# Kernel tuning notes

Hardware: AMD Instinct MI355X
Metric: run time of the kernel (lower is better)

## Reference

```python
import jax, jax.numpy as jnp
import numpy as np


def setup_inputs() -> dict:
    key = jax.random.key(0)
    ks = jax.random.split(key, 6)
    B, T, D, U = 32, 2048, 512, 512
    scale = 1.0 / np.sqrt(D)
    return {
        "values": jax.random.normal(ks[0], (B, T, D), dtype=jnp.float32),
        "query": jax.random.normal(ks[1], (B, D), dtype=jnp.float32),
        "W1": jax.random.normal(ks[2], (D, U), dtype=jnp.float32) * scale,
        "b1": jnp.zeros((U,), dtype=jnp.float32),
        "W2": jax.random.normal(ks[3], (D, U), dtype=jnp.float32) * scale,
        "b2": jnp.zeros((U,), dtype=jnp.float32),
        "V": jax.random.normal(ks[4], (U, 1), dtype=jnp.float32) * (1.0 / np.sqrt(U)),
        "bV": jnp.zeros((1,), dtype=jnp.float32),
    }


def reference(values, query, W1, b1, W2, b2, V, bV):
    # values: [B,T,D], query: [B,D]
    proj_v = jnp.einsum("btd,du->btu", values, W1) + b1          # [B,T,U]
    proj_q = (query @ W2 + b2)[:, None, :]                        # [B,1,U]
    score = jnp.tanh(proj_v + proj_q) @ V + bV                    # [B,T,1]
    attention_weights = jax.nn.softmax(score, axis=1)             # [B,T,1]
    context_vector = jnp.sum(attention_weights * values, axis=1)  # [B,D]
    return context_vector, attention_weights
```

## Files before the change

kernel.cpp:

```cpp
#include <hip/hip_runtime.h>
#include <math.h>


#define B_ 32
#define T_ 2048
#define D_ 512
#define U_ 512
#define M_ (B_ * T_)

typedef _Float16 half8 __attribute__((ext_vector_type(8)));
typedef float floatx4 __attribute__((ext_vector_type(4)));

__device__ __forceinline__ float fast_tanh(float x) {
  x = fminf(fmaxf(x, -20.f), 20.f);
  const float e = __expf(2.f * x);
  return 1.f - 2.f / (e + 1.f);
}

__device__ __forceinline__ void load_lds16f(const float* g, float* l) {
  __builtin_amdgcn_global_load_lds(
      (const __attribute__((address_space(1))) void*)g,
      (__attribute__((address_space(3))) void*)l, 16, 0, 0);
}

__global__ __launch_bounds__(256) void prep_fused(
    const float* __restrict__ W1, const float* __restrict__ query,
    const float* __restrict__ W2, const float* __restrict__ b2,
    _Float16* __restrict__ w1t, float* __restrict__ projq,
    float* __restrict__ context) {
  __shared__ float sh[64 * 65];
  const int bx = blockIdx.x;
  const int tid = threadIdx.x;
  if (bx < 64) {
    const int t = bx;
    const int k0 = (t >> 3) * 64, u0 = (t & 7) * 64;
    float(*sm)[65] = (float(*)[65])sh;
    const int lu = tid & 63;
    const int g = tid >> 6;
#pragma unroll
    for (int i = 0; i < 16; ++i) {
      const int row = g * 16 + i;
      sm[row][lu] = W1[(long)(k0 + row) * U_ + u0 + lu];
    }
    __syncthreads();
#pragma unroll
    for (int i = 0; i < 16; ++i) {
      const int row = g * 16 + i;
      w1t[(long)(u0 + row) * D_ + k0 + lu] = (_Float16)sm[lu][row];
    }
  } else {
    const int t = bx - 64;
    const int gid = t * 256 + tid;
    context[gid] = 0.f;
    const int b = t >> 1;
    const int u = (t & 1) * 256 + tid;
    for (int d = tid; d < D_; d += 256) sh[d] = query[b * D_ + d];
    __syncthreads();
    float acc = 0.f;
#pragma unroll 8
    for (int d = 0; d < D_; ++d) acc += sh[d] * W2[d * U_ + u];
    projq[b * U_ + u] = acc + b2[u];
  }
}

__global__ __launch_bounds__(512, 1) void score_fused(
    const float* __restrict__ values, const _Float16* __restrict__ w1t,
    const float* __restrict__ b1, const float* __restrict__ projq,
    const float* __restrict__ V, float* __restrict__ scores) {
  const int m0 = blockIdx.x * 128;
  const int b = blockIdx.x >> 4;
  const int tid = threadIdx.x;
  const int lane = tid & 63;
  const int w = tid >> 6;
  const int wm = (w & 1) * 64;
  const int wu = (w >> 1) * 128;
  const int ln = lane & 15;
  const int lq = lane >> 4;

  __shared__ alignas(16) float As[2][128 * 32];
  __shared__ float red[4][128];

  const int dr = lane >> 3;
  const int dc = (lane & 7) ^ dr;
  const float* gA[2];
#pragma unroll
  for (int j = 0; j < 2; ++j) {
    const int r = w * 16 + j * 8 + dr;
    gA[j] = values + (long)(m0 + r) * D_ + dc * 4;
  }

  const _Float16* bp[8];
#pragma unroll
  for (int ni = 0; ni < 8; ++ni)
    bp[ni] = w1t + (long)(wu + ni * 16 + ln) * D_ + lq * 8;

  floatx4 acc[4][8] = {};

#pragma unroll
  for (int j = 0; j < 2; ++j)
    load_lds16f(gA[j], &As[0][(w * 16 + j * 8) * 32]);
  __syncthreads();

  for (int t = 0; t < 16; ++t) {
    const int p = t & 1;
    half8 bf[8];
#pragma unroll
    for (int ni = 0; ni < 8; ++ni) bf[ni] = *(const half8*)(bp[ni] + t * 32);
    if (t < 15) {
#pragma unroll
      for (int j = 0; j < 2; ++j)
        load_lds16f(gA[j] + (t + 1) * 32,
                    &As[p ^ 1][(w * 16 + j * 8) * 32]);
    }
    half8 af[4];
#pragma unroll
    for (int mi = 0; mi < 4; ++mi) {
      const int r = wm + mi * 16 + ln;
      const float* row = &As[p][r * 32];
      const float4 lo = *(const float4*)(row + (((2 * lq) ^ (r & 7)) * 4));
      const float4 hi = *(const float4*)(row + (((2 * lq + 1) ^ (r & 7)) * 4));
      af[mi] = half8{(_Float16)lo.x, (_Float16)lo.y, (_Float16)lo.z,
                     (_Float16)lo.w, (_Float16)hi.x, (_Float16)hi.y,
                     (_Float16)hi.z, (_Float16)hi.w};
    }
#pragma unroll
    for (int mi = 0; mi < 4; ++mi)
#pragma unroll
      for (int ni = 0; ni < 8; ++ni)
        acc[mi][ni] = __builtin_amdgcn_mfma_f32_16x16x32_f16(
            af[mi], bf[ni], acc[mi][ni], 0, 0, 0);
    __syncthreads();
  }

  float pre[8], vv[8];
#pragma unroll
  for (int ni = 0; ni < 8; ++ni) {
    const int u = wu + ni * 16 + ln;
    pre[ni] = b1[u] + projq[b * U_ + u];
    vv[ni] = V[u];
  }
#pragma unroll
  for (int mi = 0; mi < 4; ++mi) {
#pragma unroll
    for (int r = 0; r < 4; ++r) {
      float t = 0.f;
#pragma unroll
      for (int ni = 0; ni < 8; ++ni)
        t += fast_tanh(acc[mi][ni][r] + pre[ni]) * vv[ni];
      t += __shfl_xor(t, 1);
      t += __shfl_xor(t, 2);
      t += __shfl_xor(t, 4);
      t += __shfl_xor(t, 8);
      if (ln == 0) red[w >> 1][wm + mi * 16 + lq * 4 + r] = t;
    }
  }
  __syncthreads();
  if (tid < 128)
    scores[m0 + tid] =
        red[0][tid] + red[1][tid] + red[2][tid] + red[3][tid];
}

__global__ __launch_bounds__(256) void softmax_context_kernel(
    const float* __restrict__ scores, const float* __restrict__ values,
    float* __restrict__ weights, float* __restrict__ context) {
  const int b = blockIdx.x;
  const int t0 = blockIdx.y * 64;
  const int tid = threadIdx.x;

  float v[8];
  float mx = -INFINITY;
#pragma unroll
  for (int i = 0; i < 8; ++i) {
    v[i] = scores[b * T_ + i * 256 + tid];
    mx = fmaxf(mx, v[i]);
  }
#pragma unroll
  for (int off = 32; off > 0; off >>= 1) mx = fmaxf(mx, __shfl_down(mx, off));
  __shared__ float sm[4], ss[4];
  if ((tid & 63) == 0) sm[tid >> 6] = mx;
  __syncthreads();
  mx = fmaxf(fmaxf(sm[0], sm[1]), fmaxf(sm[2], sm[3]));
  float sum = 0.f;
#pragma unroll
  for (int i = 0; i < 8; ++i) sum += __expf(v[i] - mx);
#pragma unroll
  for (int off = 32; off > 0; off >>= 1) sum += __shfl_down(sum, off);
  if ((tid & 63) == 0) ss[tid >> 6] = sum;
  __syncthreads();
  const float inv = 1.f / (ss[0] + ss[1] + ss[2] + ss[3]);

  __shared__ float wsh[64];
  if (tid < 64) {
    const float ww = __expf(scores[b * T_ + t0 + tid] - mx) * inv;
    wsh[tid] = ww;
    weights[b * T_ + t0 + tid] = ww;
  }
  __syncthreads();

  const int g = tid >> 7;
  const int dx = tid & 127;
  __shared__ float4 part[128];
  float4 acc = make_float4(0.f, 0.f, 0.f, 0.f);
  const float4* vp = (const float4*)(values + (long)(b * T_ + t0 + g) * D_) + dx;
#pragma unroll 4
  for (int t = 0; t < 32; ++t) {
    const float4 x = vp[(long)(2 * t) * (D_ / 4)];
    const float ww = wsh[2 * t + g];
    acc.x += ww * x.x; acc.y += ww * x.y; acc.z += ww * x.z; acc.w += ww * x.w;
  }
  if (g == 0) part[dx] = acc;
  __syncthreads();
  if (g == 1) {
    const float4 p = part[dx];
    atomicAdd(&context[b * D_ + dx * 4 + 0], acc.x + p.x);
    atomicAdd(&context[b * D_ + dx * 4 + 1], acc.y + p.y);
    atomicAdd(&context[b * D_ + dx * 4 + 2], acc.z + p.z);
    atomicAdd(&context[b * D_ + dx * 4 + 3], acc.w + p.w);
  }
}

extern "C" void kernel_launch(void* const* d_in, const int* in_sizes, int n_in,
                              void* d_out, int out_size, void* d_ws, size_t ws_size,
                              hipStream_t stream) {
  const float* values = (const float*)d_in[0];
  const float* query = (const float*)d_in[1];
  const float* W1 = (const float*)d_in[2];
  const float* b1 = (const float*)d_in[3];
  const float* W2 = (const float*)d_in[4];
  const float* b2 = (const float*)d_in[5];
  const float* V = (const float*)d_in[6];

  float* out = (float*)d_out;
  float* context = out;
  float* weights = out + B_ * D_;
  float* projq = (float*)d_ws;
  float* scores = projq + B_ * U_;
  _Float16* w1t = (_Float16*)((char*)d_ws + 65536 + 262144);

  prep_fused<<<128, 256, 0, stream>>>(W1, query, W2, b2, w1t, projq, context);
  score_fused<<<M_ / 128, 512, 0, stream>>>(values, w1t, b1, projq, V, scores);
  softmax_context_kernel<<<dim3(B_, T_ / 64), 256, 0, stream>>>(
      scores, values, weights, context);
}
```

Before: 318.9 us.

## Stage W1 fp16 tiles in LDS via async global-to-LDS loads with swizzle

Instead of each wave reading its W1 fragments straight from global memory into registers every k-step, the block now cooperatively loads the whole 512x32 fp16 W1 slice into a double-buffered, XOR-swizzled LDS tile using global_load_lds. The MFMA B operands are then read from LDS. The W1 load is also issued before the register fragment loads so it overlaps with compute. The aim is to remove duplicated global/L2 traffic for W1, since each B row was previously loaded by two waves, and to hide the load latency. The cost is 64KB of extra LDS, which brings the total to about 100KB.

```diff
diff --git a/kernel.cpp b/kernel.cpp
--- a/kernel.cpp
+++ b/kernel.cpp
@@ -18,6 +18,12 @@
 }
 
 __device__ __forceinline__ void load_lds16f(const float* g, float* l) {
+  __builtin_amdgcn_global_load_lds(
+      (const __attribute__((address_space(1))) void*)g,
+      (__attribute__((address_space(3))) void*)l, 16, 0, 0);
+}
+
+__device__ __forceinline__ void load_lds16h(const _Float16* g, _Float16* l) {
   __builtin_amdgcn_global_load_lds(
       (const __attribute__((address_space(1))) void*)g,
       (__attribute__((address_space(3))) void*)l, 16, 0, 0);
@@ -78,6 +84,7 @@
   const int lq = lane >> 4;
 
   __shared__ alignas(16) float As[2][128 * 32];
+  __shared__ alignas(16) _Float16 Bs[2][512 * 32];
   __shared__ float red[4][128];
 
   const int dr = lane >> 3;
@@ -89,28 +96,40 @@
     gA[j] = values + (long)(m0 + r) * D_ + dc * 4;
   }
 
-  const _Float16* bp[8];
-#pragma unroll
-  for (int ni = 0; ni < 8; ++ni)
-    bp[ni] = w1t + (long)(wu + ni * 16 + ln) * D_ + lq * 8;
+  const int br = lane >> 2;
+  const int bc = (lane & 3) ^ (br & 3);
+  const _Float16* gB[4];
+#pragma unroll
+  for (int i = 0; i < 4; ++i) {
+    const int r = w * 64 + i * 16 + br;
+    gB[i] = w1t + (long)r * D_ + bc * 8;
+  }
 
   floatx4 acc[4][8] = {};
 
 #pragma unroll
   for (int j = 0; j < 2; ++j)
     load_lds16f(gA[j], &As[0][(w * 16 + j * 8) * 32]);
+#pragma unroll
+  for (int i = 0; i < 4; ++i)
+    load_lds16h(gB[i], &Bs[0][(w * 64 + i * 16) * 32]);
   __syncthreads();
 
   for (int t = 0; t < 16; ++t) {
     const int p = t & 1;
+    if (t < 15) {
+#pragma unroll
+      for (int j = 0; j < 2; ++j)
+        load_lds16f(gA[j] + (t + 1) * 32, &As[p ^ 1][(w * 16 + j * 8) * 32]);
+#pragma unroll
+      for (int i = 0; i < 4; ++i)
+        load_lds16h(gB[i] + (t + 1) * 32, &Bs[p ^ 1][(w * 64 + i * 16) * 32]);
+    }
     half8 bf[8];
 #pragma unroll
-    for (int ni = 0; ni < 8; ++ni) bf[ni] = *(const half8*)(bp[ni] + t * 32);
-    if (t < 15) {
-#pragma unroll
-      for (int j = 0; j < 2; ++j)
-        load_lds16f(gA[j] + (t + 1) * 32,
-                    &As[p ^ 1][(w * 16 + j * 8) * 32]);
+    for (int ni = 0; ni < 8; ++ni) {
+      const int r = wu + ni * 16 + ln;
+      bf[ni] = *(const half8*)&Bs[p][r * 32 + ((lq ^ (ln & 3)) * 8)];
     }
     half8 af[4];
 #pragma unroll
```

Result: faster. 298.4 us (-6.4%).
